# Kernel optimization log

Measured on AMD Instinct MI355X. Metric: run time of the kernel, lower is better.

Reference implementation:

```python
import jax, jax.numpy as jnp
import numpy as np

N, K, CIN, COUT = 1_000_000, 27, 32, 32  # active voxels, 3^3 kernel offsets, channels
EPS = 1e-5


def setup_inputs() -> dict:
    key = jax.random.key(0)
    k0, k1, k2, k3 = jax.random.split(key, 4)
    feats = jax.random.normal(k0, (N, CIN), jnp.float32)
    # per-kernel-offset weight matrices, Kaiming-ish scale
    W = jax.random.normal(k1, (K, CIN, COUT), jnp.float32) * (1.0 / np.sqrt(K * CIN))
    gamma = jnp.ones((COUT,), jnp.float32)
    beta = jnp.zeros((COUT,), jnp.float32)
    # precomputed sparse-conv neighbor map: index of input voxel contributing
    nbr_idx = jax.random.randint(k2, (N, K), 0, N, jnp.int32)
    nbr_mask = jax.random.bernoulli(k3, 0.5, (N, K))
    return {"feats": feats, "W": W, "gamma": gamma, "beta": beta,
            "nbr_idx": nbr_idx, "nbr_mask": nbr_mask}


def _sparse_conv(feats, W, nbr_idx, nbr_mask):
    # gather-GEMM-scatter, looped over the small fixed kernel volume (27)
    # to avoid materializing an [N, 27, CIN] gathered tensor.
    acc = jnp.zeros((feats.shape[0], W.shape[2]), feats.dtype)
    for k in range(W.shape[0]):
        g = jnp.where(nbr_mask[:, k, None], feats[nbr_idx[:, k]], 0.0)  # [N, CIN]
        acc = acc + g @ W[k]  # [N, COUT]
    return acc


def reference(feats, W, gamma, beta, nbr_idx, nbr_mask):
    y = _sparse_conv(feats, W, nbr_idx, nbr_mask)           # conv (bias=False, bn=True)
    mean = jnp.mean(y, axis=0)                              # MinkowskiBatchNorm (batch stats)
    var = jnp.mean(jnp.square(y - mean), axis=0)
    y = (y - mean) * jax.lax.rsqrt(var + EPS) * gamma + beta
    return jax.nn.relu(y)                                   # MinkowskiReLU
```

## Files before the change

### kernel.cpp

```cpp
#include <hip/hip_runtime.h>

typedef _Float16 half8 __attribute__((ext_vector_type(8)));
typedef float floatx4 __attribute__((ext_vector_type(4)));

#define CIN 32
#define COUT 32
#define KOFF 27
#define EPSV 1e-5f


__global__ void setup_k(const float* __restrict__ W, _Float16* __restrict__ wp,
                        const unsigned char* __restrict__ m,
                        int* __restrict__ flag) {
  if (blockIdx.x < KOFF) {
    int ko = blockIdx.x;
    int h = threadIdx.x >> 6;
    int lane = threadIdx.x & 63;
    int col = lane & 15, quad = lane >> 4;
    half8 p;
#pragma unroll
    for (int j = 0; j < 8; ++j) {
      int k = quad * 8 + j;
      p[j] = (_Float16)W[(ko * CIN + k) * COUT + h * 16 + col];
    }
    *(half8*)(wp + ((size_t)(ko * 2 + h) * 64 + lane) * 8) = p;
  } else {
    int tid = threadIdx.x;
    int any = 0;
    for (int i = tid; i < 4096; i += 128) {
      if ((i & 3) != 0 && m[i] != 0) any = 1;
    }
    if (any) atomicOr(flag, 1);
  }
}

__global__ void prep_k(const float* __restrict__ feats,
                       _Float16* __restrict__ f16, int total8,
                       const unsigned char* __restrict__ nmask,
                       const int* __restrict__ flagp,
                       unsigned int* __restrict__ mpack, int N,
                       int cvtBlocks) {
  int tid = threadIdx.x;
  if ((int)blockIdx.x < cvtBlocks) {
    int t = blockIdx.x * 256 + tid;
    if (t < total8) {
      const floatx4* in4 = (const floatx4*)feats;
      floatx4 a = __builtin_nontemporal_load(&in4[(size_t)t * 2]);
      floatx4 b = __builtin_nontemporal_load(&in4[(size_t)t * 2 + 1]);
      half8 h;
      h[0] = (_Float16)a[0]; h[1] = (_Float16)a[1];
      h[2] = (_Float16)a[2]; h[3] = (_Float16)a[3];
      h[4] = (_Float16)b[0]; h[5] = (_Float16)b[1];
      h[6] = (_Float16)b[2]; h[7] = (_Float16)b[3];
      *(half8*)(f16 + (size_t)t * 8) = h;
    } else if (t < total8 + 4) {
      half8 z;
#pragma unroll
      for (int j = 0; j < 8; ++j) z[j] = (_Float16)0.f;
      *(half8*)(f16 + (size_t)t * 8) = z;
    }
  } else {
    int vox = (blockIdx.x - cvtBlocks) * 256 + tid;
    if (vox >= N) return;
    unsigned int mk = 0;
    if (*flagp != 0) {
      const unsigned char* p = nmask + (size_t)vox * KOFF;
#pragma unroll
      for (int ko = 0; ko < KOFF; ++ko)
        mk |= (p[ko] != 0 ? 1u : 0u) << ko;
    } else {
      const int* p = (const int*)nmask + (size_t)vox * KOFF;
#pragma unroll
      for (int ko = 0; ko < KOFF; ++ko)
        mk |= (p[ko] != 0 ? 1u : 0u) << ko;
    }
    mpack[vox] = mk;
  }
}

__launch_bounds__(256, 3)
__global__ void conv_mfma_d(const _Float16* __restrict__ f16,
                            const _Float16* __restrict__ wp,
                            const int* __restrict__ nidx,
                            const unsigned int* __restrict__ mpack,
                            float* __restrict__ y,
                            float* __restrict__ stats, int N) {
  __shared__ float smS[4 * 32];
  __shared__ float smQ[4 * 32];
  int wave = threadIdx.x >> 6;
  int lane = threadIdx.x & 63;
  int base = (blockIdx.x * 4 + wave) * 64;
  bool active = base < N;
  int col = lane & 15, quad = lane >> 4;
  const half8* wfrag = (const half8*)wp;
  const _Float16* fq = f16 + quad * 8;

  floatx4 acc[4][2];
#pragma unroll
  for (int t = 0; t < 4; ++t)
#pragma unroll
    for (int h = 0; h < 2; ++h) {
      acc[t][h][0] = 0.f; acc[t][h][1] = 0.f;
      acc[t][h][2] = 0.f; acc[t][h][3] = 0.f;
    }

  if (active) {
    unsigned int mp[4];
    int o27[4];
#pragma unroll
    for (int t = 0; t < 4; ++t) {
      int vox = base + t * 16 + col;
      if (vox > N - 1) vox = N - 1;
      o27[t] = vox * KOFF;
      mp[t] = mpack[vox];
    }
    int ivB[4];
    half8 aC[4];
#pragma unroll
    for (int t = 0; t < 4; ++t) {
      int iv0 = nidx[o27[t]];
      int sel = (mp[t] & 1u) ? iv0 : N;
      aC[t] = *(const half8*)(fq + ((size_t)sel << 5));
    }
#pragma unroll
    for (int t = 0; t < 4; ++t) ivB[t] = nidx[o27[t] + 1];
    half8 bC0 = wfrag[lane];
    half8 bC1 = wfrag[64 + lane];

#pragma unroll
    for (int ko = 0; ko < KOFF; ++ko) {
      int ivN[4];
      if (ko + 2 < KOFF) {
#pragma unroll
        for (int t = 0; t < 4; ++t) ivN[t] = nidx[o27[t] + ko + 2];
      }
      half8 bN0, bN1;
      if (ko + 1 < KOFF) {
        bN0 = wfrag[(size_t)((ko + 1) * 2 + 0) * 64 + lane];
        bN1 = wfrag[(size_t)((ko + 1) * 2 + 1) * 64 + lane];
      }
      half8 aN[4];
      if (ko + 1 < KOFF) {
#pragma unroll
        for (int t = 0; t < 4; ++t) {
          int sel = ((mp[t] >> (ko + 1)) & 1u) ? ivB[t] : N;
          aN[t] = *(const half8*)(fq + ((size_t)sel << 5));
        }
      }
#pragma unroll
      for (int t = 0; t < 4; ++t) {
        acc[t][0] = __builtin_amdgcn_mfma_f32_16x16x32_f16(aC[t], bC0, acc[t][0], 0, 0, 0);
        acc[t][1] = __builtin_amdgcn_mfma_f32_16x16x32_f16(aC[t], bC1, acc[t][1], 0, 0, 0);
      }
      if (ko + 1 < KOFF) {
#pragma unroll
        for (int t = 0; t < 4; ++t) aC[t] = aN[t];
        bC0 = bN0; bC1 = bN1;
      }
      if (ko + 2 < KOFF) {
#pragma unroll
        for (int t = 0; t < 4; ++t) ivB[t] = ivN[t];
      }
    }
  }

  float s0 = 0.f, s1 = 0.f, q0 = 0.f, q1 = 0.f;
  if (active) {
#pragma unroll
    for (int t = 0; t < 4; ++t) {
#pragma unroll
      for (int h = 0; h < 2; ++h) {
        floatx4 c = acc[t][h];
        int co = h * 16 + col;
#pragma unroll
        for (int r = 0; r < 4; ++r) {
          int vox = base + t * 16 + quad * 4 + r;
          if (vox < N) {
            y[(size_t)vox * COUT + co] = c[r];
            float v = c[r];
            if (h == 0) { s0 += v; q0 += v * v; }
            else        { s1 += v; q1 += v * v; }
          }
        }
      }
    }
  }
  s0 += __shfl_xor(s0, 16); s0 += __shfl_xor(s0, 32);
  s1 += __shfl_xor(s1, 16); s1 += __shfl_xor(s1, 32);
  q0 += __shfl_xor(q0, 16); q0 += __shfl_xor(q0, 32);
  q1 += __shfl_xor(q1, 16); q1 += __shfl_xor(q1, 32);
  if (quad == 0) {
    smS[wave * 32 + col] = s0;
    smS[wave * 32 + 16 + col] = s1;
    smQ[wave * 32 + col] = q0;
    smQ[wave * 32 + 16 + col] = q1;
  }
  __syncthreads();
  int tid = threadIdx.x;
  if (tid < 64) {
    int co = tid & 31;
    const float* arr = (tid < 32) ? smS : smQ;
    float s = arr[co] + arr[32 + co] + arr[64 + co] + arr[96 + co];
    atomicAdd(&stats[(tid < 32 ? 0 : 32) + co], s);
  }
}

__global__ void bn_apply(float* __restrict__ y, const float* __restrict__ stats,
                         const float* __restrict__ gamma,
                         const float* __restrict__ beta, int total4, float invN) {
  __shared__ float sc_sh[64];
  int tid = threadIdx.x;
  if (tid < 32) {
    float mean = stats[tid] * invN;
    float ex2 = stats[32 + tid] * invN;
    float var = ex2 - mean * mean;
    float inv = rsqrtf(var + EPSV);
    float sc = gamma[tid] * inv;
    sc_sh[tid] = sc;
    sc_sh[32 + tid] = beta[tid] - mean * sc;
  }
  __syncthreads();
  int t = blockIdx.x * blockDim.x + tid;
  if (t >= total4) return;
  size_t g = (size_t)t * 4;
  int co = (int)(g & 31);
  floatx4 v = *(const floatx4*)(y + g);
  floatx4 sc = *(const floatx4*)&sc_sh[co];
  floatx4 sh = *(const floatx4*)&sc_sh[32 + co];
  floatx4 o;
#pragma unroll
  for (int j = 0; j < 4; ++j) o[j] = fmaxf(0.f, v[j] * sc[j] + sh[j]);
  __builtin_nontemporal_store(o, (floatx4*)(y + g));
}

extern "C" void kernel_launch(void* const* d_in, const int* in_sizes, int n_in,
                              void* d_out, int out_size, void* d_ws,
                              size_t ws_size, hipStream_t stream) {
  const float* feats = (const float*)d_in[0];
  const float* W = (const float*)d_in[1];
  const float* gamma = (const float*)d_in[2];
  const float* beta = (const float*)d_in[3];
  const int* nidx = (const int*)d_in[4];
  const unsigned char* nmask = (const unsigned char*)d_in[5];
  float* out = (float*)d_out;

  int N = in_sizes[0] / CIN;

  char* ws = (char*)d_ws;
  size_t f16_bytes = (size_t)(N + 1) * CIN * sizeof(_Float16);
  _Float16* f16 = (_Float16*)ws;
  _Float16* wp = (_Float16*)(ws + f16_bytes);
  size_t wp_bytes = (size_t)KOFF * 2 * 64 * 8 * sizeof(_Float16);
  size_t stats_off = ((f16_bytes + wp_bytes + 511) / 512) * 512;
  float* stats = (float*)(ws + stats_off);
  int* flag = (int*)(stats + 64);
  size_t mpack_off = ((stats_off + 768 + 255) / 256) * 256;
  unsigned int* mpack = (unsigned int*)(ws + mpack_off);

  hipMemsetAsync(stats, 0, 65 * sizeof(float), stream);

  setup_k<<<KOFF + 1, 128, 0, stream>>>(W, wp, nmask, flag);

  int total8 = N * CIN / 8;
  int cvtBlocks = (total8 + 4 + 255) / 256;
  int mkBlocks = (N + 255) / 256;
  prep_k<<<cvtBlocks + mkBlocks, 256, 0, stream>>>(feats, f16, total8, nmask,
                                                   flag, mpack, N, cvtBlocks);

  int nwaves = (N + 63) / 64;
  int nblocks = (nwaves + 3) / 4;
  conv_mfma_d<<<nblocks, 256, 0, stream>>>(f16, wp, nidx, mpack, out, stats, N);

  int total4 = N * COUT / 4;
  bn_apply<<<(total4 + 255) / 256, 256, 0, stream>>>(out, stats, gamma, beta,
                                                     total4, 1.0f / (float)N);
}
```

Before: 683.3 us.

## Stage neighbor indices and masks in LDS with coalesced loads, drop mask-pack pass

The conv kernel now loads each wave's 64x27 neighbor indices and masks with coalesced int4 loads into shared memory and folds the mask bit into the index sign bit. This replaces the earlier strided per-lane global index loads and removes the separate mask-packing pass in prep_k along with its mpack buffer. It uses about 27KB of LDS per block while raising the launch-bounds occupancy hint from 3 to 4 blocks. Folding the mask into bit 31 assumes indices are non-negative and below 2^31.

```diff
diff --git a/kernel.cpp b/kernel.cpp
--- a/kernel.cpp
+++ b/kernel.cpp
@@ -35,56 +35,35 @@
 }
 
 __global__ void prep_k(const float* __restrict__ feats,
-                       _Float16* __restrict__ f16, int total8,
-                       const unsigned char* __restrict__ nmask,
-                       const int* __restrict__ flagp,
-                       unsigned int* __restrict__ mpack, int N,
-                       int cvtBlocks) {
-  int tid = threadIdx.x;
-  if ((int)blockIdx.x < cvtBlocks) {
-    int t = blockIdx.x * 256 + tid;
-    if (t < total8) {
-      const floatx4* in4 = (const floatx4*)feats;
-      floatx4 a = __builtin_nontemporal_load(&in4[(size_t)t * 2]);
-      floatx4 b = __builtin_nontemporal_load(&in4[(size_t)t * 2 + 1]);
-      half8 h;
-      h[0] = (_Float16)a[0]; h[1] = (_Float16)a[1];
-      h[2] = (_Float16)a[2]; h[3] = (_Float16)a[3];
-      h[4] = (_Float16)b[0]; h[5] = (_Float16)b[1];
-      h[6] = (_Float16)b[2]; h[7] = (_Float16)b[3];
-      *(half8*)(f16 + (size_t)t * 8) = h;
-    } else if (t < total8 + 4) {
-      half8 z;
-#pragma unroll
-      for (int j = 0; j < 8; ++j) z[j] = (_Float16)0.f;
-      *(half8*)(f16 + (size_t)t * 8) = z;
-    }
-  } else {
-    int vox = (blockIdx.x - cvtBlocks) * 256 + tid;
-    if (vox >= N) return;
-    unsigned int mk = 0;
-    if (*flagp != 0) {
-      const unsigned char* p = nmask + (size_t)vox * KOFF;
-#pragma unroll
-      for (int ko = 0; ko < KOFF; ++ko)
-        mk |= (p[ko] != 0 ? 1u : 0u) << ko;
-    } else {
-      const int* p = (const int*)nmask + (size_t)vox * KOFF;
-#pragma unroll
-      for (int ko = 0; ko < KOFF; ++ko)
-        mk |= (p[ko] != 0 ? 1u : 0u) << ko;
-    }
-    mpack[vox] = mk;
-  }
-}
-
-__launch_bounds__(256, 3)
-__global__ void conv_mfma_d(const _Float16* __restrict__ f16,
+                       _Float16* __restrict__ f16, int total8) {
+  int t = blockIdx.x * 256 + threadIdx.x;
+  if (t < total8) {
+    const floatx4* in4 = (const floatx4*)feats;
+    floatx4 a = __builtin_nontemporal_load(&in4[(size_t)t * 2]);
+    floatx4 b = __builtin_nontemporal_load(&in4[(size_t)t * 2 + 1]);
+    half8 h;
+    h[0] = (_Float16)a[0]; h[1] = (_Float16)a[1];
+    h[2] = (_Float16)a[2]; h[3] = (_Float16)a[3];
+    h[4] = (_Float16)b[0]; h[5] = (_Float16)b[1];
+    h[6] = (_Float16)b[2]; h[7] = (_Float16)b[3];
+    *(half8*)(f16 + (size_t)t * 8) = h;
+  } else if (t < total8 + 4) {
+    half8 z;
+#pragma unroll
+    for (int j = 0; j < 8; ++j) z[j] = (_Float16)0.f;
+    *(half8*)(f16 + (size_t)t * 8) = z;
+  }
+}
+
+__launch_bounds__(256, 4)
+__global__ void conv_mfma_l(const _Float16* __restrict__ f16,
                             const _Float16* __restrict__ wp,
                             const int* __restrict__ nidx,
-                            const unsigned int* __restrict__ mpack,
+                            const unsigned char* __restrict__ nmask,
+                            const int* __restrict__ flagp,
                             float* __restrict__ y,
                             float* __restrict__ stats, int N) {
+  __shared__ int lidx[4 * 64 * KOFF];
   __shared__ float smS[4 * 32];
   __shared__ float smQ[4 * 32];
   int wave = threadIdx.x >> 6;
@@ -94,6 +73,7 @@
   int col = lane & 15, quad = lane >> 4;
   const half8* wfrag = (const half8*)wp;
   const _Float16* fq = f16 + quad * 8;
+  int* lw = lidx + wave * (64 * KOFF);
 
   floatx4 acc[4][2];
 #pragma unroll
@@ -105,47 +85,77 @@
     }
 
   if (active) {
-    unsigned int mp[4];
-    int o27[4];
+    bool bytemode = (*flagp != 0);
+    int nv = N - base; if (nv > 64) nv = 64;
+    if (nv == 64) {
+      const int4* gi = (const int4*)(nidx + (size_t)base * KOFF);
+      const int4* gm4 = (const int4*)((const int*)nmask + (size_t)base * KOFF);
+      const unsigned int* gmb = (const unsigned int*)(nmask + (size_t)base * KOFF);
+#pragma unroll
+      for (int s = 0; s < 7; ++s) {
+        int id4 = s * 64 + lane;
+        if (id4 < 432) {
+          int4 iv = gi[id4];
+          unsigned int m0, m1, m2, m3;
+          if (bytemode) {
+            unsigned int mw = gmb[id4];
+            m0 = mw & 0xffu; m1 = mw & 0xff00u;
+            m2 = mw & 0xff0000u; m3 = mw & 0xff000000u;
+          } else {
+            int4 mv = gm4[id4];
+            m0 = (unsigned int)mv.x; m1 = (unsigned int)mv.y;
+            m2 = (unsigned int)mv.z; m3 = (unsigned int)mv.w;
+          }
+          int4 ov;
+          ov.x = (iv.x & 0x7FFFFFFF) | (m0 ? (int)0x80000000 : 0);
+          ov.y = (iv.y & 0x7FFFFFFF) | (m1 ? (int)0x80000000 : 0);
+          ov.z = (iv.z & 0x7FFFFFFF) | (m2 ? (int)0x80000000 : 0);
+          ov.w = (iv.w & 0x7FFFFFFF) | (m3 ? (int)0x80000000 : 0);
+          *(int4*)(lw + id4 * 4) = ov;
+        }
+      }
+    } else {
+      int total = nv * KOFF;
+      for (int p = lane; p < total; p += 64) {
+        size_t g = (size_t)base * KOFF + p;
+        int iv = nidx[g];
+        int mk = bytemode ? (int)nmask[g] : ((const int*)nmask)[g];
+        lw[p] = (iv & 0x7FFFFFFF) | (mk ? (int)0x80000000 : 0);
+      }
+      for (int p = nv * KOFF + lane; p < 64 * KOFF; p += 64) lw[p] = 0;
+    }
+
+    half8 aC[4];
+    int ivB[4];
 #pragma unroll
     for (int t = 0; t < 4; ++t) {
-      int vox = base + t * 16 + col;
-      if (vox > N - 1) vox = N - 1;
-      o27[t] = vox * KOFF;
-      mp[t] = mpack[vox];
-    }
-    int ivB[4];
-    half8 aC[4];
-#pragma unroll
-    for (int t = 0; t < 4; ++t) {
-      int iv0 = nidx[o27[t]];
-      int sel = (mp[t] & 1u) ? iv0 : N;
+      int v0 = lw[(t * 16 + col) * KOFF + 0];
+      int sel = (v0 < 0) ? (v0 & 0x7FFFFFFF) : N;
       aC[t] = *(const half8*)(fq + ((size_t)sel << 5));
-    }
-#pragma unroll
-    for (int t = 0; t < 4; ++t) ivB[t] = nidx[o27[t] + 1];
+      ivB[t] = lw[(t * 16 + col) * KOFF + 1];
+    }
     half8 bC0 = wfrag[lane];
     half8 bC1 = wfrag[64 + lane];
 
 #pragma unroll
     for (int ko = 0; ko < KOFF; ++ko) {
+      half8 aN[4];
+      half8 bN0, bN1;
       int ivN[4];
-      if (ko + 2 < KOFF) {
-#pragma unroll
-        for (int t = 0; t < 4; ++t) ivN[t] = nidx[o27[t] + ko + 2];
-      }
-      half8 bN0, bN1;
       if (ko + 1 < KOFF) {
         bN0 = wfrag[(size_t)((ko + 1) * 2 + 0) * 64 + lane];
         bN1 = wfrag[(size_t)((ko + 1) * 2 + 1) * 64 + lane];
-      }
-      half8 aN[4];
-      if (ko + 1 < KOFF) {
 #pragma unroll
         for (int t = 0; t < 4; ++t) {
-          int sel = ((mp[t] >> (ko + 1)) & 1u) ? ivB[t] : N;
+          int v = ivB[t];
+          int sel = (v < 0) ? (v & 0x7FFFFFFF) : N;
           aN[t] = *(const half8*)(fq + ((size_t)sel << 5));
         }
+      }
+      if (ko + 2 < KOFF) {
+#pragma unroll
+        for (int t = 0; t < 4; ++t)
+          ivN[t] = lw[(t * 16 + col) * KOFF + ko + 2];
       }
 #pragma unroll
       for (int t = 0; t < 4; ++t) {
@@ -254,8 +264,6 @@
   size_t stats_off = ((f16_bytes + wp_bytes + 511) / 512) * 512;
   float* stats = (float*)(ws + stats_off);
   int* flag = (int*)(stats + 64);
-  size_t mpack_off = ((stats_off + 768 + 255) / 256) * 256;
-  unsigned int* mpack = (unsigned int*)(ws + mpack_off);
 
   hipMemsetAsync(stats, 0, 65 * sizeof(float), stream);
 
@@ -263,13 +271,12 @@
 
   int total8 = N * CIN / 8;
   int cvtBlocks = (total8 + 4 + 255) / 256;
-  int mkBlocks = (N + 255) / 256;
-  prep_k<<<cvtBlocks + mkBlocks, 256, 0, stream>>>(feats, f16, total8, nmask,
-                                                   flag, mpack, N, cvtBlocks);
+  prep_k<<<cvtBlocks, 256, 0, stream>>>(feats, f16, total8);
 
   int nwaves = (N + 63) / 64;
   int nblocks = (nwaves + 3) / 4;
-  conv_mfma_d<<<nblocks, 256, 0, stream>>>(f16, wp, nidx, mpack, out, stats, N);
+  conv_mfma_l<<<nblocks, 256, 0, stream>>>(f16, wp, nidx, nmask, flag, out,
+                                           stats, N);
 
   int total4 = N * COUT / 4;
   bn_apply<<<(total4 + 255) / 256, 256, 0, stream>>>(out, stats, gamma, beta,
```

Measured after the change: 623.1 us. 8.8% less time.
